# Kernel optimization log

Measured on AMD Instinct MI355X. Metric: run time of the kernel, lower is better.

Reference implementation:

```python
import jax, jax.numpy as jnp
import numpy as np
import math

B, H, S, D = 2, 16, 2048, 64
MASK_NEG = -1e9


def setup_inputs() -> dict:
    key = jax.random.key(0)
    kq, kk, kv, kc, km = jax.random.split(key, 5)
    q = jax.random.normal(kq, (B, H, S, D), dtype=jnp.float32)
    k = jax.random.normal(kk, (B, H, S, D), dtype=jnp.float32)
    v = jax.random.normal(kv, (B, H, S, D), dtype=jnp.float32)
    constant = jax.random.normal(kc, (1, H, 1, 1), dtype=jnp.float32)
    mask = jax.random.randint(km, (B, S), 0, 2, dtype=jnp.int32)  # 1 = masked out
    return {"q": q, "k": k, "v": v, "constant": constant, "mask": mask}


def leaky_softmax(x, leaky_factor):
    # custom 'leaky' softmax: denominator gets an extra exp(c - max) * S term
    m = jnp.max(x, axis=-1, keepdims=True)
    exp_x = jnp.exp(x - m)
    leak = jnp.exp(leaky_factor - m) * x.shape[-1]
    return exp_x / (jnp.sum(exp_x, axis=-1, keepdims=True) + leak)


def reference(q, k, v, constant, mask):
    scale = jnp.float32(1.0 / math.sqrt(q.shape[-1]))
    # scores: [B,H,S,S]
    scores = jnp.einsum("bhqd,bhkd->bhqk", q, k) * scale
    m = mask.astype(q.dtype)[:, None, None, :]  # [B,1,1,S]
    scores = scores + m * MASK_NEG
    probs = leaky_softmax(scores, constant)
    out = jnp.einsum("bhqk,bhkd->bhqd", probs, v)
    return out, probs
```

## Files before the change

### kernel.cpp

```cpp
#include <hip/hip_runtime.h>
#include <hip/hip_bf16.h>
#include <cstdint>
#include <cstddef>

#define BB 2
#define HH 16
#define SS 2048
#define DD 64
#define NBH (BB * HH)
#define BQ 16
#define NWAVES 8
#define BLK 512
#define CW 512
#define NCHUNK (SS / CW)
#define CSTRIDE 516

typedef __attribute__((ext_vector_type(8))) short bf16x8;
typedef __attribute__((ext_vector_type(4))) float f32x4;
typedef __attribute__((ext_vector_type(4))) unsigned short us4;

#define LGKM_BAR() asm volatile("s_waitcnt lgkmcnt(0)\n\ts_barrier" ::: "memory")

__device__ __forceinline__ unsigned short f2bf(float x) {
  union { float f; uint32_t u; } c;
  c.f = x;
  uint32_t u = c.u;
  uint32_t r = (u + 0x7FFFu + ((u >> 16) & 1u)) >> 16;
  return (unsigned short)r;
}

__global__ __launch_bounds__(256) void cvt_qk_kernel(
    const float* __restrict__ q, const float* __restrict__ k,
    unsigned short* __restrict__ qb, unsigned short* __restrict__ kb) {
  size_t i = ((size_t)blockIdx.x * 256 + threadIdx.x) * 4;
  float4 a = *(const float4*)(q + i);
  float4 b = *(const float4*)(k + i);
  us4 qa = {f2bf(a.x), f2bf(a.y), f2bf(a.z), f2bf(a.w)};
  us4 ka = {f2bf(b.x), f2bf(b.y), f2bf(b.z), f2bf(b.w)};
  *(us4*)(qb + i) = qa;
  *(us4*)(kb + i) = ka;
}

__global__ __launch_bounds__(256) void cvt_vt_kernel(
    const float* __restrict__ v, unsigned short* __restrict__ vt) {
  __shared__ unsigned short t[64][65];
  const int tid = threadIdx.x;
  const int bh = blockIdx.y;
  const int s0 = blockIdx.x * 64;
  const float* vb = v + ((size_t)bh * SS + s0) * DD;
#pragma unroll
  for (int it = 0; it < 16; ++it) {
    int idx = it * 256 + tid;
    int s = idx >> 6, d = idx & 63;
    t[s][d] = f2bf(vb[idx]);
  }
  __syncthreads();
  unsigned short* vo = vt + (size_t)bh * DD * SS + s0;
#pragma unroll
  for (int it = 0; it < 16; ++it) {
    int idx = it * 256 + tid;
    int d = idx >> 6, s = idx & 63;
    vo[(size_t)d * SS + s] = t[s][d];
  }
}

__global__ __launch_bounds__(BLK, 4) void attn_kernel(
    const unsigned short* __restrict__ qb,
    const unsigned short* __restrict__ kb,
    const unsigned short* __restrict__ vt,
    const float* __restrict__ cst,
    const int* __restrict__ mask,
    float* __restrict__ out,
    float* __restrict__ probs) {
  __shared__ float pch[BQ][CSTRIDE];
  __shared__ float stats[NWAVES][BQ];
  __shared__ float rowinv[BQ];

  const int tid = threadIdx.x;
  const int wave = tid >> 6;
  const int lane = tid & 63;
  const int quad = lane >> 4;
  const int l16 = lane & 15;
  const int bh = blockIdx.y;
  const int bidx = bh >> 4;
  const int h = bh & 15;
  const int q0 = blockIdx.x * BQ;

  const unsigned short* qrow = qb + ((size_t)bh * SS + q0 + l16) * DD + quad * 8;
  bf16x8 aq0 = *(const bf16x8*)(qrow);
  bf16x8 aq1 = *(const bf16x8*)(qrow + 32);

  const unsigned short* kbase = kb + (size_t)bh * SS * DD;
  const int* mrow = mask + bidx * SS;

  float rsum[4] = {0.f, 0.f, 0.f, 0.f};
#pragma unroll
  for (int t = 0; t < 16; ++t) {
    int col0 = (wave + 8 * t) * 16;
    const unsigned short* krow = kbase + (size_t)(col0 + l16) * DD + quad * 8;
    bf16x8 bk0 = *(const bf16x8*)(krow);
    bf16x8 bk1 = *(const bf16x8*)(krow + 32);
    f32x4 c = {0.f, 0.f, 0.f, 0.f};
    c = __builtin_amdgcn_mfma_f32_16x16x32_bf16(aq0, bk0, c, 0, 0, 0);
    c = __builtin_amdgcn_mfma_f32_16x16x32_bf16(aq1, bk1, c, 0, 0, 0);
    int mk = mrow[col0 + l16];
#pragma unroll
    for (int r = 0; r < 4; ++r)
      rsum[r] += mk ? 0.0f : __expf(c[r] * 0.125f);
  }
#pragma unroll
  for (int off = 8; off >= 1; off >>= 1)
#pragma unroll
    for (int r = 0; r < 4; ++r)
      rsum[r] += __shfl_xor(rsum[r], off, 64);
  if (l16 == 0)
#pragma unroll
    for (int r = 0; r < 4; ++r) stats[wave][quad * 4 + r] = rsum[r];
  __syncthreads();
  if (tid < BQ) {
    float s = 0.f;
#pragma unroll
    for (int w = 0; w < NWAVES; ++w) s += stats[w][tid];
    float denom = s + __expf(cst[h]) * (float)SS;
    rowinv[tid] = 1.0f / denom;
  }
  __syncthreads();
  float inv[4];
#pragma unroll
  for (int r = 0; r < 4; ++r) inv[r] = rowinv[quad * 4 + r];

  f32x4 acco[4];
#pragma unroll
  for (int dt = 0; dt < 4; ++dt) acco[dt] = (f32x4){0.f, 0.f, 0.f, 0.f};
  const unsigned short* vbase = vt + (size_t)bh * DD * SS;
#pragma unroll
  for (int c = 0; c < NCHUNK; ++c) {
    const int kg0 = c * CW + wave * 64 + quad * 8;
    bf16x8 v0[4];
#pragma unroll
    for (int dt = 0; dt < 4; ++dt)
      v0[dt] = *(const bf16x8*)(vbase + (size_t)(dt * 16 + l16) * SS + kg0);

    if (c) LGKM_BAR();
#pragma unroll
    for (int tt = 0; tt < 4; ++tt) {
      int t = c * 4 + tt;
      int col0 = (wave + 8 * t) * 16;
      const unsigned short* krow = kbase + (size_t)(col0 + l16) * DD + quad * 8;
      bf16x8 bk0 = *(const bf16x8*)(krow);
      bf16x8 bk1 = *(const bf16x8*)(krow + 32);
      f32x4 ct = {0.f, 0.f, 0.f, 0.f};
      ct = __builtin_amdgcn_mfma_f32_16x16x32_bf16(aq0, bk0, ct, 0, 0, 0);
      ct = __builtin_amdgcn_mfma_f32_16x16x32_bf16(aq1, bk1, ct, 0, 0, 0);
      int mk = mrow[col0 + l16];
      int lcol = tt * 128 + wave * 16 + l16;
#pragma unroll
      for (int r = 0; r < 4; ++r) {
        float e = mk ? 0.0f : __expf(ct[r] * 0.125f) * inv[r];
        pch[quad * 4 + r][lcol] = e;
      }
    }
    LGKM_BAR();

    {
      const f32x4* ap4 = (const f32x4*)&pch[l16][wave * 64 + quad * 8];
      f32x4 p0 = ap4[0], p1 = ap4[1];
      union { bf16x8 v8; uint32_t u[4]; } apu;
      asm("v_cvt_pk_bf16_f32 %0, %1, %2" : "=v"(apu.u[0]) : "v"(p0.x), "v"(p0.y));
      asm("v_cvt_pk_bf16_f32 %0, %1, %2" : "=v"(apu.u[1]) : "v"(p0.z), "v"(p0.w));
      asm("v_cvt_pk_bf16_f32 %0, %1, %2" : "=v"(apu.u[2]) : "v"(p1.x), "v"(p1.y));
      asm("v_cvt_pk_bf16_f32 %0, %1, %2" : "=v"(apu.u[3]) : "v"(p1.z), "v"(p1.w));
      bf16x8 ap = apu.v8;
      bf16x8 v1[4];
#pragma unroll
      for (int dt = 0; dt < 4; ++dt)
        v1[dt] = *(const bf16x8*)(vbase + (size_t)(dt * 16 + l16) * SS + kg0 + 32);
#pragma unroll
      for (int dt = 0; dt < 4; ++dt)
        acco[dt] = __builtin_amdgcn_mfma_f32_16x16x32_bf16(ap, v0[dt], acco[dt], 0, 0, 0);

      const f32x4* bp4 = (const f32x4*)&pch[l16][wave * 64 + 32 + quad * 8];
      f32x4 q0v = bp4[0], q1v = bp4[1];
      union { bf16x8 v8; uint32_t u[4]; } bpu;
      asm("v_cvt_pk_bf16_f32 %0, %1, %2" : "=v"(bpu.u[0]) : "v"(q0v.x), "v"(q0v.y));
      asm("v_cvt_pk_bf16_f32 %0, %1, %2" : "=v"(bpu.u[1]) : "v"(q0v.z), "v"(q0v.w));
      asm("v_cvt_pk_bf16_f32 %0, %1, %2" : "=v"(bpu.u[2]) : "v"(q1v.x), "v"(q1v.y));
      asm("v_cvt_pk_bf16_f32 %0, %1, %2" : "=v"(bpu.u[3]) : "v"(q1v.z), "v"(q1v.w));
      bf16x8 bp = bpu.v8;
#pragma unroll
      for (int dt = 0; dt < 4; ++dt)
        acco[dt] = __builtin_amdgcn_mfma_f32_16x16x32_bf16(bp, v1[dt], acco[dt], 0, 0, 0);
    }

#pragma unroll
    for (int i = 0; i < 4; ++i) {
      int f = i * BLK + tid;
      int row = f >> 7, c4 = f & 127;
      f32x4 val = *(const f32x4*)&pch[row][c4 * 4];
      f32x4* dst = (f32x4*)(probs + (size_t)bh * SS * SS +
                            (size_t)(q0 + row) * SS + c * CW) + c4;
      __builtin_nontemporal_store(val, dst);
    }
  }

  LGKM_BAR();
  float* outp = &pch[0][0];
#pragma unroll
  for (int dt = 0; dt < 4; ++dt)
#pragma unroll
    for (int r = 0; r < 4; ++r)
      outp[((wave * BQ) + quad * 4 + r) * DD + dt * 16 + l16] = acco[dt][r];
  LGKM_BAR();
  for (int e = tid; e < BQ * DD; e += BLK) {
    int row = e >> 6, col = e & 63;
    float s = 0.f;
#pragma unroll
    for (int w = 0; w < NWAVES; ++w) s += outp[(w * BQ + row) * DD + col];
    out[((size_t)bh * SS + q0 + row) * DD + col] = s;
  }
}

extern "C" void kernel_launch(void* const* d_in, const int* in_sizes, int n_in,
                              void* d_out, int out_size, void* d_ws, size_t ws_size,
                              hipStream_t stream) {
  const float* q = (const float*)d_in[0];
  const float* k = (const float*)d_in[1];
  const float* v = (const float*)d_in[2];
  const float* cst = (const float*)d_in[3];
  const int* mask = (const int*)d_in[4];

  float* out = (float*)d_out;
  float* probs = out + (size_t)NBH * SS * DD;

  const size_t nelem = (size_t)NBH * SS * DD;
  unsigned short* qb = (unsigned short*)d_ws;
  unsigned short* kb = qb + nelem;
  unsigned short* vt = kb + nelem;

  cvt_qk_kernel<<<dim3((unsigned)(nelem / (256 * 4))), 256, 0, stream>>>(q, k, qb, kb);
  cvt_vt_kernel<<<dim3(SS / 64, NBH), 256, 0, stream>>>(v, vt);

  attn_kernel<<<dim3(SS / BQ, NBH), BLK, 0, stream>>>(qb, kb, vt, cst, mask, out, probs);
}
```

Before: 865.9 us.

## Halve LDS chunk width and software-pipeline K/V loads and probs stores

Shrinks the probability chunk from 512 to 256 columns, which roughly halves the LDS footprint per block. K and V fragments for the next chunk are now prefetched into registers while the current chunk is processed. Mask bits are cached in a bitmask during the first pass so the second pass does not reload them. Probs are read from LDS into registers before the next chunk's loads are issued, with a sched barrier to order global stores after the prefetches. The output reduction is split into two halves so it fits the smaller LDS buffer. In exchange, the kernel makes twice as many chunk iterations and barriers, and holds more registers for the prefetched fragments.

```diff
diff --git a/kernel.cpp b/kernel.cpp
--- a/kernel.cpp
+++ b/kernel.cpp
@@ -11,9 +11,9 @@
 #define BQ 16
 #define NWAVES 8
 #define BLK 512
-#define CW 512
+#define CW 256
 #define NCHUNK (SS / CW)
-#define CSTRIDE 516
+#define CSTRIDE 260
 
 typedef __attribute__((ext_vector_type(8))) short bf16x8;
 typedef __attribute__((ext_vector_type(4))) float f32x4;
@@ -94,6 +94,7 @@
   const int* mrow = mask + bidx * SS;
 
   float rsum[4] = {0.f, 0.f, 0.f, 0.f};
+  unsigned int mbits = 0;
 #pragma unroll
   for (int t = 0; t < 16; ++t) {
     int col0 = (wave + 8 * t) * 16;
@@ -104,6 +105,7 @@
     c = __builtin_amdgcn_mfma_f32_16x16x32_bf16(aq0, bk0, c, 0, 0, 0);
     c = __builtin_amdgcn_mfma_f32_16x16x32_bf16(aq1, bk1, c, 0, 0, 0);
     int mk = mrow[col0 + l16];
+    mbits |= (unsigned)(mk & 1) << t;
 #pragma unroll
     for (int r = 0; r < 4; ++r)
       rsum[r] += mk ? 0.0f : __expf(c[r] * 0.125f);
@@ -133,37 +135,41 @@
 #pragma unroll
   for (int dt = 0; dt < 4; ++dt) acco[dt] = (f32x4){0.f, 0.f, 0.f, 0.f};
   const unsigned short* vbase = vt + (size_t)bh * DD * SS;
+
+  bf16x8 kpref[4];
+  bf16x8 vpref[4];
+  f32x4 sreg[2][2];
+
+#pragma unroll
+  for (int tt = 0; tt < 2; ++tt) {
+    int col0 = (8 * tt + wave) * 16;
+    const unsigned short* krow = kbase + (size_t)(col0 + l16) * DD + quad * 8;
+    kpref[2 * tt] = *(const bf16x8*)(krow);
+    kpref[2 * tt + 1] = *(const bf16x8*)(krow + 32);
+  }
+#pragma unroll
+  for (int dt = 0; dt < 4; ++dt)
+    vpref[dt] = *(const bf16x8*)(vbase + (size_t)(dt * 16 + l16) * SS +
+                                 wave * 32 + quad * 8);
+
 #pragma unroll
   for (int c = 0; c < NCHUNK; ++c) {
-    const int kg0 = c * CW + wave * 64 + quad * 8;
-    bf16x8 v0[4];
-#pragma unroll
-    for (int dt = 0; dt < 4; ++dt)
-      v0[dt] = *(const bf16x8*)(vbase + (size_t)(dt * 16 + l16) * SS + kg0);
-
     if (c) LGKM_BAR();
 #pragma unroll
-    for (int tt = 0; tt < 4; ++tt) {
-      int t = c * 4 + tt;
-      int col0 = (wave + 8 * t) * 16;
-      const unsigned short* krow = kbase + (size_t)(col0 + l16) * DD + quad * 8;
-      bf16x8 bk0 = *(const bf16x8*)(krow);
-      bf16x8 bk1 = *(const bf16x8*)(krow + 32);
+    for (int tt = 0; tt < 2; ++tt) {
       f32x4 ct = {0.f, 0.f, 0.f, 0.f};
-      ct = __builtin_amdgcn_mfma_f32_16x16x32_bf16(aq0, bk0, ct, 0, 0, 0);
-      ct = __builtin_amdgcn_mfma_f32_16x16x32_bf16(aq1, bk1, ct, 0, 0, 0);
-      int mk = mrow[col0 + l16];
-      int lcol = tt * 128 + wave * 16 + l16;
-#pragma unroll
-      for (int r = 0; r < 4; ++r) {
-        float e = mk ? 0.0f : __expf(ct[r] * 0.125f) * inv[r];
-        pch[quad * 4 + r][lcol] = e;
-      }
+      ct = __builtin_amdgcn_mfma_f32_16x16x32_bf16(aq0, kpref[2 * tt], ct, 0, 0, 0);
+      ct = __builtin_amdgcn_mfma_f32_16x16x32_bf16(aq1, kpref[2 * tt + 1], ct, 0, 0, 0);
+      int mk = (int)((mbits >> (2 * c + tt)) & 1u);
+      int lcol = (8 * tt + wave) * 16 + l16;
+#pragma unroll
+      for (int r = 0; r < 4; ++r)
+        pch[quad * 4 + r][lcol] = mk ? 0.0f : __expf(ct[r] * 0.125f) * inv[r];
     }
     LGKM_BAR();
 
     {
-      const f32x4* ap4 = (const f32x4*)&pch[l16][wave * 64 + quad * 8];
+      const f32x4* ap4 = (const f32x4*)&pch[l16][wave * 32 + quad * 8];
       f32x4 p0 = ap4[0], p1 = ap4[1];
       union { bf16x8 v8; uint32_t u[4]; } apu;
       asm("v_cvt_pk_bf16_f32 %0, %1, %2" : "=v"(apu.u[0]) : "v"(p0.x), "v"(p0.y));
@@ -171,52 +177,62 @@
       asm("v_cvt_pk_bf16_f32 %0, %1, %2" : "=v"(apu.u[2]) : "v"(p1.x), "v"(p1.y));
       asm("v_cvt_pk_bf16_f32 %0, %1, %2" : "=v"(apu.u[3]) : "v"(p1.z), "v"(p1.w));
       bf16x8 ap = apu.v8;
-      bf16x8 v1[4];
 #pragma unroll
       for (int dt = 0; dt < 4; ++dt)
-        v1[dt] = *(const bf16x8*)(vbase + (size_t)(dt * 16 + l16) * SS + kg0 + 32);
+        acco[dt] = __builtin_amdgcn_mfma_f32_16x16x32_bf16(ap, vpref[dt], acco[dt], 0, 0, 0);
+    }
+
+#pragma unroll
+    for (int i = 0; i < 2; ++i) {
+      int f = i * BLK + tid;
+      int row = f >> 6, c4 = f & 63;
+      sreg[c & 1][i] = *(const f32x4*)&pch[row][c4 * 4];
+    }
+
+    if (c + 1 < NCHUNK) {
+#pragma unroll
+      for (int tt = 0; tt < 2; ++tt) {
+        int col0 = (16 * (c + 1) + 8 * tt + wave) * 16;
+        const unsigned short* krow = kbase + (size_t)(col0 + l16) * DD + quad * 8;
+        kpref[2 * tt] = *(const bf16x8*)(krow);
+        kpref[2 * tt + 1] = *(const bf16x8*)(krow + 32);
+      }
+      int kg = (c + 1) * CW + wave * 32 + quad * 8;
 #pragma unroll
       for (int dt = 0; dt < 4; ++dt)
-        acco[dt] = __builtin_amdgcn_mfma_f32_16x16x32_bf16(ap, v0[dt], acco[dt], 0, 0, 0);
-
-      const f32x4* bp4 = (const f32x4*)&pch[l16][wave * 64 + 32 + quad * 8];
-      f32x4 q0v = bp4[0], q1v = bp4[1];
-      union { bf16x8 v8; uint32_t u[4]; } bpu;
-      asm("v_cvt_pk_bf16_f32 %0, %1, %2" : "=v"(bpu.u[0]) : "v"(q0v.x), "v"(q0v.y));
-      asm("v_cvt_pk_bf16_f32 %0, %1, %2" : "=v"(bpu.u[1]) : "v"(q0v.z), "v"(q0v.w));
-      asm("v_cvt_pk_bf16_f32 %0, %1, %2" : "=v"(bpu.u[2]) : "v"(q1v.x), "v"(q1v.y));
-      asm("v_cvt_pk_bf16_f32 %0, %1, %2" : "=v"(bpu.u[3]) : "v"(q1v.z), "v"(q1v.w));
-      bf16x8 bp = bpu.v8;
-#pragma unroll
-      for (int dt = 0; dt < 4; ++dt)
-        acco[dt] = __builtin_amdgcn_mfma_f32_16x16x32_bf16(bp, v1[dt], acco[dt], 0, 0, 0);
-    }
-
-#pragma unroll
-    for (int i = 0; i < 4; ++i) {
+        vpref[dt] = *(const bf16x8*)(vbase + (size_t)(dt * 16 + l16) * SS + kg);
+    }
+    __builtin_amdgcn_sched_barrier(0);
+
+#pragma unroll
+    for (int i = 0; i < 2; ++i) {
       int f = i * BLK + tid;
-      int row = f >> 7, c4 = f & 127;
-      f32x4 val = *(const f32x4*)&pch[row][c4 * 4];
+      int row = f >> 6, c4 = f & 63;
       f32x4* dst = (f32x4*)(probs + (size_t)bh * SS * SS +
                             (size_t)(q0 + row) * SS + c * CW) + c4;
-      __builtin_nontemporal_store(val, dst);
+      __builtin_nontemporal_store(sreg[c & 1][i], dst);
     }
   }
 
   LGKM_BAR();
   float* outp = &pch[0][0];
 #pragma unroll
-  for (int dt = 0; dt < 4; ++dt)
-#pragma unroll
-    for (int r = 0; r < 4; ++r)
-      outp[((wave * BQ) + quad * 4 + r) * DD + dt * 16 + l16] = acco[dt][r];
-  LGKM_BAR();
-  for (int e = tid; e < BQ * DD; e += BLK) {
-    int row = e >> 6, col = e & 63;
-    float s = 0.f;
-#pragma unroll
-    for (int w = 0; w < NWAVES; ++w) s += outp[(w * BQ + row) * DD + col];
-    out[((size_t)bh * SS + q0 + row) * DD + col] = s;
+  for (int half = 0; half < 2; ++half) {
+    if (half) LGKM_BAR();
+#pragma unroll
+    for (int dt = 0; dt < 2; ++dt)
+#pragma unroll
+      for (int r = 0; r < 4; ++r)
+        outp[((wave * BQ) + quad * 4 + r) * 32 + dt * 16 + l16] =
+            acco[half * 2 + dt][r];
+    LGKM_BAR();
+    for (int e = tid; e < BQ * 32; e += BLK) {
+      int row = e >> 5, col = e & 31;
+      float s = 0.f;
+#pragma unroll
+      for (int w = 0; w < NWAVES; ++w) s += outp[(w * BQ + row) * 32 + col];
+      out[((size_t)bh * SS + q0 + row) * DD + half * 32 + col] = s;
+    }
   }
 }
 
```

New measurement: 849.7 us. No clear change (-1.9%).
